# Kernel tuning notes

Hardware: AMD Instinct MI355X
Metric: run time of the kernel (lower is better)

## Reference

```python
import jax, jax.numpy as jnp
import numpy as np

E, H, V, B, T = 256, 512, 50257, 4, 512
EPS = 1e-5  # torch F.layer_norm default


def _ln(x):
    m = jnp.mean(x, axis=-1, keepdims=True)
    v = jnp.var(x, axis=-1, keepdims=True)
    return (x - m) / jnp.sqrt(v + EPS)


def setup_inputs() -> dict:
    key = jax.random.key(0)
    ks = iter(jax.random.split(key, 40))

    def w(shape):
        return jax.random.normal(next(ks), shape, dtype=jnp.float32) * 0.02

    inp = {"input_ids": jax.random.randint(next(ks), (B, T), 0, V)}
    inp["emb_table"] = w((V, E))
    for i, e in [(0, E), (1, H)]:  # layer 0 input = emb_dim, layer 1 input = hidden_dim
        inp[f"Wc1_{i}"] = w((2 * H + e, 2 * H)); inp[f"bc1_{i}"] = w((2 * H,))
        inp[f"Wc2_{i}"] = w((2 * H, H));         inp[f"bc2_{i}"] = w((H,))
        inp[f"Wg1_{i}"] = w((2 * H + e, H));     inp[f"bg1_{i}"] = w((H,))
        inp[f"Wg2_{i}"] = w((H, 1));             inp[f"bg2_{i}"] = w((1,))
        inp[f"Wr_{i}"] = w((e, H));              inp[f"br_{i}"] = w((H,))
    inp["Wa1"] = w((H, H)); inp["ba1"] = w((H,))
    inp["Wa2"] = w((H, 1)); inp["ba2"] = w((1,))
    inp["Wh"] = w((H, V));  inp["bh"] = w((V,))
    return inp


def _forward(input_ids, emb_table,
             Wc1_0, bc1_0, Wc2_0, bc2_0, Wg1_0, bg1_0, Wg2_0, bg2_0, Wr_0, br_0,
             Wc1_1, bc1_1, Wc2_1, bc2_1, Wg1_1, bg1_1, Wg2_1, bg2_1, Wr_1, br_1,
             Wa1, ba1, Wa2, ba2, Wh, bh):
    layers = [
        (Wc1_0, bc1_0, Wc2_0, bc2_0, Wg1_0, bg1_0, Wg2_0, bg2_0, Wr_0, br_0),
        (Wc1_1, bc1_1, Wc2_1, bc2_1, Wg1_1, bg1_1, Wg2_1, bg2_1, Wr_1, br_1),
    ]
    emb = emb_table[input_ids]  # [B,T,E]

    def step(carry, x_t):
        h2s, h1s = carry  # tuples of [B,H] per layer
        new_h2, new_h1 = [], []
        inp = x_t
        gate = None
        for (Wc1, bc1, Wc2, bc2, Wg1, bg1, Wg2, bg2, Wr, br), h2, h1 in zip(layers, h2s, h1s):
            ctx = jnp.concatenate([h1, h2, inp], axis=-1)  # [B, 2H+e]
            cand = jnp.maximum(ctx @ Wc1 + bc1, 0.0) @ Wc2 + bc2
            gate = jax.nn.sigmoid(jnp.tanh(ctx @ Wg1 + bg1) @ Wg2 + bg2)[:, 0]  # [B]
            h = _ln(h1 + gate[:, None] * cand + 0.1 * (inp @ Wr + br))
            new_h2.append(h1); new_h1.append(h)
            inp = h
        return (tuple(new_h2), tuple(new_h1)), (inp, gate)

    z = jnp.zeros((B, H), emb.dtype)
    init = ((z, z), (z, z))
    _, (hist, gates) = jax.lax.scan(step, init, jnp.swapaxes(emb, 0, 1))
    hist = jnp.swapaxes(hist, 0, 1)    # [B,T,H] last-layer hidden states
    gates = jnp.swapaxes(gates, 0, 1)  # [B,T]

    # Additive attention over the growing prefix: scores are fixed per position,
    # so prefix-softmax context = cumsum(exp(s)*h) / cumsum(exp(s)).
    scores = (jnp.tanh(hist @ Wa1 + ba1) @ Wa2 + ba2)[..., 0]  # [B,T]
    m = jnp.max(scores, axis=1, keepdims=True)
    e = jnp.exp(scores - m)
    num = jnp.cumsum(e[..., None] * hist, axis=1)  # [B,T,H]
    den = jnp.cumsum(e, axis=1)[..., None]
    attended = hist + num / den
    logits = attended @ Wh + bh  # [B,T,V]
    return logits, gates


def reference(input_ids, emb_table,
              Wc1_0, bc1_0, Wc2_0, bc2_0, Wg1_0, bg1_0, Wg2_0, bg2_0, Wr_0, br_0,
              Wc1_1, bc1_1, Wc2_1, bc2_1, Wg1_1, bg1_1, Wg2_1, bg2_1, Wr_1, br_1,
              Wa1, ba1, Wa2, ba2, Wh, bh):
    return _forward(input_ids, emb_table,
                    Wc1_0, bc1_0, Wc2_0, bc2_0, Wg1_0, bg1_0, Wg2_0, bg2_0, Wr_0, br_0,
                    Wc1_1, bc1_1, Wc2_1, bc2_1, Wg1_1, bg1_1, Wg2_1, bg2_1, Wr_1, br_1,
                    Wa1, ba1, Wa2, ba2, Wh, bh)
```

## Files before the change

### kernel.cpp

```cpp
#include <hip/hip_runtime.h>
#include <hip/hip_fp16.h>
#include <cstdint>
#include <cstddef>

typedef unsigned short u16;
typedef unsigned int   u32;
typedef unsigned long long u64;

#define Bn 4
#define Tn 512
#define Hn 512
#define En 256
#define Vn 50257
#define NPAD 50304
#define RG  256
#define RNT 256

typedef _Float16 h2t __attribute__((ext_vector_type(2)));

#if defined(__has_builtin)
#if __has_builtin(__builtin_amdgcn_fdot2)
#define HAS_FDOT2 1
#endif
#endif
__device__ __forceinline__ float fdot2f(h2t a, h2t b, float c) {
#ifdef HAS_FDOT2
  return __builtin_amdgcn_fdot2(a, b, c, false);
#else
  return fmaf((float)a[0], (float)b[0], fmaf((float)a[1], (float)b[1], c));
#endif
}

__device__ __forceinline__ u16 f2bf(float f) {
  u32 x; __builtin_memcpy(&x, &f, 4);
  u32 r = (x + 0x7fffu + ((x >> 16) & 1u)) >> 16;
  return (u16)r;
}
__device__ __forceinline__ u16 f2h(float f) {
  __half hh = __float2half(f); u16 u; __builtin_memcpy(&u, &hh, 2); return u;
}
__device__ __forceinline__ float h2fu(u16 h) {
  __half hh; __builtin_memcpy(&hh, &h, 2); return __half2float(hh);
}
__device__ __forceinline__ u64 gldu64(const u64* p) {
  return __hip_atomic_load(p, __ATOMIC_RELAXED, __HIP_MEMORY_SCOPE_AGENT);
}
__device__ __forceinline__ void gstu64(u64* p, u64 v) {
  __hip_atomic_store(p, v, __ATOMIC_RELAXED, __HIP_MEMORY_SCOPE_AGENT);
}
__device__ __forceinline__ u32 gldu32(const u32* p) {
  return __hip_atomic_load(p, __ATOMIC_RELAXED, __HIP_MEMORY_SCOPE_AGENT);
}
__device__ __forceinline__ void gstu32(u32* p, u32 v) {
  __hip_atomic_store(p, v, __ATOMIC_RELAXED, __HIP_MEMORY_SCOPE_AGENT);
}
__device__ __forceinline__ void gstf(float* p, float v) {
  __hip_atomic_store(p, v, __ATOMIC_RELAXED, __HIP_MEMORY_SCOPE_AGENT);
}

__global__ __launch_bounds__(256) void transpose_h(
    const float* __restrict__ src, __half* __restrict__ dst, int K, int N)
{
  __shared__ float tile[32][33];
  const int tx = threadIdx.x & 31, ty = threadIdx.x >> 5;
  const int bn = blockIdx.x * 32, bk = blockIdx.y * 32;
  #pragma unroll
  for (int i = 0; i < 4; ++i)
    tile[ty + i * 8][tx] = src[(size_t)(bk + ty + i * 8) * N + bn + tx];
  __syncthreads();
  #pragma unroll
  for (int i = 0; i < 4; ++i)
    dst[(size_t)(bn + ty + i * 8) * K + bk + tx] = __float2half(tile[tx][ty + i * 8]);
}

__global__ __launch_bounds__(256) void convwh_kernel(
    const float* __restrict__ wh, u16* __restrict__ whb)
{
  const int k = blockIdx.y;
  const int v0 = (blockIdx.x * 256 + threadIdx.x) * 2;
  if (v0 >= NPAD) return;
  float a = (v0     < Vn) ? wh[(size_t)k * Vn + v0]     : 0.f;
  float b = (v0 + 1 < Vn) ? wh[(size_t)k * Vn + v0 + 1] : 0.f;
  u32 pack = (u32)f2bf(a) | ((u32)f2bf(b) << 16);
  *(u32*)&whb[(size_t)k * NPAD + v0] = pack;
}

#define HR16_B  98304
#define HR0_B   102400
#define EMB_B   104448
#define XCAND_B 105472
#define GP_B    109568
#define RLOC_B  110080
#define SS_B    110144
#define BC1L_B  110464
#define BG1L_B  110528
#define BC2L_B  110560
#define BRL_B   110592
#define WG2L_B  110624
#define BG2L_B  110656
#define REC_LDS 110720

__global__ __launch_bounds__(RNT, 1) void rec_kernel(
    const int* __restrict__ ids, const float* __restrict__ emb,
    const __half* wtC1_0, const __half* wtG1_0, const __half* wtC2_0, const __half* wtR_0,
    const __half* wtC1_1, const __half* wtG1_1, const __half* wtC2_1, const __half* wtR_1,
    const float* bc1_0, const float* bg1_0, const float* bc2_0, const float* br_0,
    const float* wg2_0, const float* bg2_0,
    const float* bc1_1, const float* bg1_1, const float* bc2_1, const float* br_1,
    const float* wg2_1, const float* bg2_1,
    u32* flagA, u64* HB, u64* CB,
    float* __restrict__ histN, float* __restrict__ gates_out)
{
  extern __shared__ char smem[];
  __half* WL    = (__half*)smem;
  __half* hr16  = (__half*)(smem + HR16_B);
  __half* hr0   = (__half*)(smem + HR0_B);
  __half* emb16 = (__half*)(smem + EMB_B);
  __half* xcand = (__half*)(smem + XCAND_B);
  float* gp     = (float*)(smem + GP_B);
  float* rloc   = (float*)(smem + RLOC_B);
  float* Ss     = (float*)(smem + SS_B);
  float* bc1L   = (float*)(smem + BC1L_B);
  float* bg1L   = (float*)(smem + BG1L_B);
  float* bc2L   = (float*)(smem + BC2L_B);
  float* brL    = (float*)(smem + BRL_B);
  float* wg2L   = (float*)(smem + WG2L_B);
  float* bg2L   = (float*)(smem + BG2L_B);

  const int tid = threadIdx.x, g = blockIdx.x;
  const int bp = g >> 7, l = (g >> 6) & 1, gl = g & 63;
  const int w = tid >> 6, lane = tid & 63;
  const int C = l ? 1536 : 1280;
  const int e = l ? 512 : 256;
  const int oG1 = 16 * C, oR = 24 * C, oC2 = 24 * C + 8 * e;

  const __half* wtC1 = l ? wtC1_1 : wtC1_0;
  const __half* wtG1 = l ? wtG1_1 : wtG1_0;
  const __half* wtC2 = l ? wtC2_1 : wtC2_0;
  const __half* wtR  = l ? wtR_1  : wtR_0;
  const float* bc1 = l ? bc1_1 : bc1_0;
  const float* bg1 = l ? bg1_1 : bg1_0;
  const float* bc2 = l ? bc2_1 : bc2_0;
  const float* br  = l ? br_1  : br_0;
  const float* wg2 = l ? wg2_1 : wg2_0;
  const float* bg2 = l ? bg2_1 : bg2_0;

  u64* HBown = HB + (size_t)((bp * 2 + l) * 2) * 512;
  u64* CBown = CB + (size_t)((bp * 2 + l) * 2) * 1152;
  const u64* HBl0 = HB + (size_t)((bp * 2) * 2) * 512;

  {
    auto cp = [&](const __half* src, int nh, int offh) {
      const u32* s = (const u32*)src; u32* d = (u32*)(WL + offh);
      for (int i = tid; i < (nh >> 1); i += RNT) d[i] = s[i];
    };
    cp(wtC1 + (size_t)(gl * 16) * C, 16 * C, 0);
    cp(wtG1 + (size_t)(gl * 8) * C,  8 * C, oG1);
    cp(wtR  + (size_t)(gl * 8) * e,  8 * e, oR);
    cp(wtC2 + (size_t)(gl * 8) * 1024, 8 * 1024, oC2);
  }
  for (int i = tid; i < 2960; i += RNT) ((u32*)(smem + HR16_B))[i] = 0;
  __syncthreads();

  if (tid < 16)      bc1L[tid] = bc1[gl * 16 + tid];
  else if (tid < 24) bg1L[tid - 16] = bg1[gl * 8 + tid - 16];
  else if (tid < 32) bc2L[tid - 24] = bc2[gl * 8 + tid - 24];
  else if (tid < 40) brL[tid - 32]  = br[gl * 8 + tid - 32];
  else if (tid < 48) wg2L[tid - 40] = wg2[gl * 8 + tid - 40];
  else if (tid == 48) bg2L[0] = bg2[0];
  for (int task = w; task < 32; task += 4) {
    const __half* colp; int K;
    if (task < 16)      { colp = WL + (size_t)task * C;              K = C; }
    else if (task < 24) { colp = WL + oG1 + (size_t)(task - 16) * C; K = C; }
    else                { colp = WL + oR  + (size_t)(task - 24) * e; K = e; }
    float s1 = 0.f, s2 = 0.f, s3 = 0.f;
    for (int k = lane; k < K; k += 64) {
      float v = __half2float(colp[k]);
      if (K == e) s1 += v;
      else if (k < 512) s1 += v;
      else if (k < 1024) s2 += v;
      else s3 += v;
    }
    #pragma unroll
    for (int off = 32; off; off >>= 1) {
      s1 += __shfl_xor(s1, off); s2 += __shfl_xor(s2, off); s3 += __shfl_xor(s3, off);
    }
    if (lane == 0) {
      if (task < 16)      { Ss[task] = s1; Ss[16 + task] = s2; Ss[32 + task] = s3; }
      else if (task < 24) { Ss[48 + task - 16] = s1; Ss[56 + task - 16] = s2; Ss[64 + task - 16] = s3; }
      else                { Ss[72 + task - 24] = s1; }
    }
  }
  __syncthreads();

  const int nEnd = l ? (Tn + 1) : (Tn - 1);
  float mp[2] = {0.f, 0.f}, ipv[2] = {0.f, 0.f};

  for (int n = 0; n <= nEnd; ++n) {
    const int t = n - l;
    const bool prod = (t >= 0) && (t < Tn);
    const bool pollOwn = (t >= 1) && (t <= Tn);
    const bool pollL0  = (l == 1) && prod;
    const int parR = (n - 1) & 1;

    float2 e2 = make_float2(0.f, 0.f);
    if (l == 0 && prod) {
      int idv = ids[(bp * 2 + (w >> 1)) * Tn + t];
      e2 = *(const float2*)(emb + (size_t)idv * En + (tid & 127) * 2);
    }

    if (pollOwn || pollL0) {
      const u64* s1 = HBown + (size_t)parR * 512;
      const u64* s0 = HBl0 + (size_t)parR * 512;
      const u32 want = (u32)n;
      u64 v1[2], v0[2];
      for (;;) {
        bool ok = true;
        if (pollOwn) { v1[0] = gldu64(s1 + tid); v1[1] = gldu64(s1 + 256 + tid); }
        if (pollL0)  { v0[0] = gldu64(s0 + tid); v0[1] = gldu64(s0 + 256 + tid); }
        if (pollOwn) ok &= ((u32)(v1[0] >> 32) == want) & ((u32)(v1[1] >> 32) == want);
        if (pollL0)  ok &= ((u32)(v0[0] >> 32) == want) & ((u32)(v0[1] >> 32) == want);
        if (ok) break;
        __builtin_amdgcn_s_sleep(1);
      }
      if (pollOwn) {
        #pragma unroll
        for (int i = 0; i < 2; ++i) {
          int W = i * 256 + tid;
          int glp = W >> 3, q = W & 7, cpp = q >> 1, b = q & 1;
          ((u32*)(hr16 + (parR * 2 + b) * 512))[glp * 4 + cpp] = (u32)v1[i];
        }
      }
      if (pollL0) {
        #pragma unroll
        for (int i = 0; i < 2; ++i) {
          int W = i * 256 + tid;
          int glp = W >> 3, q = W & 7, cpp = q >> 1, b = q & 1;
          ((u32*)(hr0 + b * 512))[glp * 4 + cpp] = (u32)v0[i];
        }
      }
    }
    if (l == 0 && prod) {
      u32 pp = (u32)f2h(e2.x) | ((u32)f2h(e2.y) << 16);
      ((u32*)emb16)[(w >> 1) * 128 + (tid & 127)] = pp;
    }
    __syncthreads();
    if (l == 1 && tid == 0) gstu32(flagA + (bp * 64 + gl) * 16, (u32)(n + 1));

    float m1[2] = {0.f, 0.f}, i1v[2] = {0.f, 0.f};
    float m3[2] = {0.f, 0.f}, i3v[2] = {0.f, 0.f};
    if (pollOwn) {
      float s[2] = {0.f, 0.f}, q[2] = {0.f, 0.f};
      #pragma unroll
      for (int b = 0; b < 2; ++b) {
        const u32* hp = (const u32*)(hr16 + (parR * 2 + b) * 512);
        #pragma unroll
        for (int i2 = 0; i2 < 4; ++i2) {
          u32 vv = hp[lane + i2 * 64];
          __half2 hh; __builtin_memcpy(&hh, &vv, 4);
          float2 f2 = __half22float2(hh);
          s[b] += f2.x + f2.y; q[b] += f2.x * f2.x + f2.y * f2.y;
        }
      }
      #pragma unroll
      for (int off = 32; off; off >>= 1) {
        s[0] += __shfl_xor(s[0], off); q[0] += __shfl_xor(q[0], off);
        s[1] += __shfl_xor(s[1], off); q[1] += __shfl_xor(q[1], off);
      }
      #pragma unroll
      for (int b = 0; b < 2; ++b) {
        float m = s[b] * (1.f / 512.f);
        m1[b] = m; i1v[b] = rsqrtf(q[b] * (1.f / 512.f) - m * m + 1e-5f);
      }
    }
    if (pollL0) {
      float s[2] = {0.f, 0.f}, q[2] = {0.f, 0.f};
      #pragma unroll
      for (int b = 0; b < 2; ++b) {
        const u32* hp = (const u32*)(hr0 + b * 512);
        #pragma unroll
        for (int i2 = 0; i2 < 4; ++i2) {
          u32 vv = hp[lane + i2 * 64];
          __half2 hh; __builtin_memcpy(&hh, &vv, 4);
          float2 f2 = __half22float2(hh);
          s[b] += f2.x + f2.y; q[b] += f2.x * f2.x + f2.y * f2.y;
        }
      }
      #pragma unroll
      for (int off = 32; off; off >>= 1) {
        s[0] += __shfl_xor(s[0], off); q[0] += __shfl_xor(q[0], off);
        s[1] += __shfl_xor(s[1], off); q[1] += __shfl_xor(q[1], off);
      }
      #pragma unroll
      for (int b = 0; b < 2; ++b) {
        float m = s[b] * (1.f / 512.f);
        m3[b] = m; i3v[b] = rsqrtf(q[b] * (1.f / 512.f) - m * m + 1e-5f);
      }
    }

    if (l == 1 && pollOwn && tid < 16) {
      int c = tid >> 1, b = tid & 1, j = gl * 8 + c;
      float rv = __half2float(hr16[(parR * 2 + b) * 512 + j]);
      gstf(histN + ((size_t)((bp * 2 + b) * Tn + (t - 1))) * Hn + j, (rv - m1[b]) * i1v[b]);
    }

    if (prod) {
      float comb[8][2];
      #pragma unroll
      for (int c = 0; c < 8; ++c) { comb[c][0] = 0.f; comb[c][1] = 0.f; }
      const __half* h1p[2] = { hr16 + (parR * 2) * 512, hr16 + (parR * 2 + 1) * 512 };
      const __half* h2p[2] = { hr16 + ((parR ^ 1) * 2) * 512, hr16 + ((parR ^ 1) * 2 + 1) * 512 };
      float a[8][2];

      if (w < 3) {
        const __half* wbase = (w < 2) ? (WL + (size_t)(w * 8) * C) : (WL + oG1);
        #pragma unroll
        for (int c = 0; c < 8; ++c) { a[c][0] = 0.f; a[c][1] = 0.f; }
        #pragma unroll
        for (int it = 0; it < 4; ++it) {
          int p2 = lane + it * 64;
          h2t x0 = *(const h2t*)(h1p[0] + 2 * p2);
          h2t x1 = *(const h2t*)(h1p[1] + 2 * p2);
          #pragma unroll
          for (int c = 0; c < 8; ++c) {
            h2t wv = *(const h2t*)(wbase + (size_t)c * C + 2 * p2);
            a[c][0] = fdot2f(wv, x0, a[c][0]);
            a[c][1] = fdot2f(wv, x1, a[c][1]);
          }
        }
        #pragma unroll
        for (int c = 0; c < 8; ++c) { comb[c][0] += i1v[0] * a[c][0]; comb[c][1] += i1v[1] * a[c][1]; }
        #pragma unroll
        for (int c = 0; c < 8; ++c) { a[c][0] = 0.f; a[c][1] = 0.f; }
        #pragma unroll
        for (int it = 0; it < 4; ++it) {
          int p2 = lane + it * 64;
          h2t x0 = *(const h2t*)(h2p[0] + 2 * p2);
          h2t x1 = *(const h2t*)(h2p[1] + 2 * p2);
          #pragma unroll
          for (int c = 0; c < 8; ++c) {
            h2t wv = *(const h2t*)(wbase + (size_t)c * C + 512 + 2 * p2);
            a[c][0] = fdot2f(wv, x0, a[c][0]);
            a[c][1] = fdot2f(wv, x1, a[c][1]);
          }
        }
        #pragma unroll
        for (int c = 0; c < 8; ++c) { comb[c][0] += ipv[0] * a[c][0]; comb[c][1] += ipv[1] * a[c][1]; }
        #pragma unroll
        for (int c = 0; c < 8; ++c) { a[c][0] = 0.f; a[c][1] = 0.f; }
        if (l == 0) {
          #pragma unroll
          for (int it = 0; it < 2; ++it) {
            int p2 = lane + it * 64;
            h2t x0 = *(const h2t*)(emb16 + 2 * p2);
            h2t x1 = *(const h2t*)(emb16 + 256 + 2 * p2);
            #pragma unroll
            for (int c = 0; c < 8; ++c) {
              h2t wv = *(const h2t*)(wbase + (size_t)c * C + 1024 + 2 * p2);
              a[c][0] = fdot2f(wv, x0, a[c][0]);
              a[c][1] = fdot2f(wv, x1, a[c][1]);
            }
          }
          #pragma unroll
          for (int c = 0; c < 8; ++c) { comb[c][0] += a[c][0]; comb[c][1] += a[c][1]; }
        } else {
          #pragma unroll
          for (int it = 0; it < 4; ++it) {
            int p2 = lane + it * 64;
            h2t x0 = *(const h2t*)(hr0 + 2 * p2);
            h2t x1 = *(const h2t*)(hr0 + 512 + 2 * p2);
            #pragma unroll
            for (int c = 0; c < 8; ++c) {
              h2t wv = *(const h2t*)(wbase + (size_t)c * C + 1024 + 2 * p2);
              a[c][0] = fdot2f(wv, x0, a[c][0]);
              a[c][1] = fdot2f(wv, x1, a[c][1]);
            }
          }
          #pragma unroll
          for (int c = 0; c < 8; ++c) { comb[c][0] += i3v[0] * a[c][0]; comb[c][1] += i3v[1] * a[c][1]; }
        }
      } else {
        #pragma unroll
        for (int c = 0; c < 8; ++c) { a[c][0] = 0.f; a[c][1] = 0.f; }
        if (l == 0) {
          #pragma unroll
          for (int it = 0; it < 2; ++it) {
            int p2 = lane + it * 64;
            h2t x0 = *(const h2t*)(emb16 + 2 * p2);
            h2t x1 = *(const h2t*)(emb16 + 256 + 2 * p2);
            #pragma unroll
            for (int c = 0; c < 8; ++c) {
              h2t wv = *(const h2t*)(WL + oR + (size_t)c * e + 2 * p2);
              a[c][0] = fdot2f(wv, x0, a[c][0]);
              a[c][1] = fdot2f(wv, x1, a[c][1]);
            }
          }
          #pragma unroll
          for (int c = 0; c < 8; ++c) { comb[c][0] = a[c][0]; comb[c][1] = a[c][1]; }
        } else {
          #pragma unroll
          for (int it = 0; it < 4; ++it) {
            int p2 = lane + it * 64;
            h2t x0 = *(const h2t*)(hr0 + 2 * p2);
            h2t x1 = *(const h2t*)(hr0 + 512 + 2 * p2);
            #pragma unroll
            for (int c = 0; c < 8; ++c) {
              h2t wv = *(const h2t*)(WL + oR + (size_t)c * e + 2 * p2);
              a[c][0] = fdot2f(wv, x0, a[c][0]);
              a[c][1] = fdot2f(wv, x1, a[c][1]);
            }
          }
          #pragma unroll
          for (int c = 0; c < 8; ++c) { comb[c][0] = i3v[0] * a[c][0]; comb[c][1] = i3v[1] * a[c][1]; }
        }
      }
      #pragma unroll
      for (int off = 32; off; off >>= 1)
        #pragma unroll
        for (int c = 0; c < 8; ++c) {
          comb[c][0] += __shfl_xor(comb[c][0], off);
          comb[c][1] += __shfl_xor(comb[c][1], off);
        }
      float v0s = 0.f, v1s = 0.f;
      #pragma unroll
      for (int c = 0; c < 8; ++c)
        if (lane == c) { v0s = comb[c][0]; v1s = comb[c][1]; }

      const u64 tagw = ((u64)(u32)(n + 1)) << 32;
      u64* CBw = CBown + (size_t)(n & 1) * 1152 + gl * 18;
      if (w < 2) {
        if (lane < 8) {
          int cg = w * 8 + lane;
          float k0 = i1v[0] * m1[0] * Ss[cg] + ipv[0] * mp[0] * Ss[16 + cg];
          float k1 = i1v[1] * m1[1] * Ss[cg] + ipv[1] * mp[1] * Ss[16 + cg];
          if (l) { k0 += i3v[0] * m3[0] * Ss[32 + cg]; k1 += i3v[1] * m3[1] * Ss[32 + cg]; }
          float bb = bc1L[cg];
          float c0 = fmaxf(v0s - k0 + bb, 0.f), c1 = fmaxf(v1s - k1 + bb, 0.f);
          u32 pay = (u32)f2h(c0) | ((u32)f2h(c1) << 16);
          gstu64(CBw + cg, tagw | pay);
        }
      } else if (w == 2) {
        if (lane < 8) {
          float k0 = i1v[0] * m1[0] * Ss[48 + lane] + ipv[0] * mp[0] * Ss[56 + lane];
          float k1 = i1v[1] * m1[1] * Ss[48 + lane] + ipv[1] * mp[1] * Ss[56 + lane];
          if (l) { k0 += i3v[0] * m3[0] * Ss[64 + lane]; k1 += i3v[1] * m3[1] * Ss[64 + lane]; }
          float bgv = bg1L[lane], wgv = wg2L[lane];
          float t0 = tanhf(v0s - k0 + bgv) * wgv;
          float t1 = tanhf(v1s - k1 + bgv) * wgv;
          #pragma unroll
          for (int off = 1; off < 8; off <<= 1) { t0 += __shfl_xor(t0, off); t1 += __shfl_xor(t1, off); }
          if (lane == 0) {
            u32 b0, b1; __builtin_memcpy(&b0, &t0, 4); __builtin_memcpy(&b1, &t1, 4);
            gstu64(CBw + 16, tagw | b0);
            gstu64(CBw + 17, tagw | b1);
          }
        }
      } else {
        if (lane < 8) {
          float k0 = l ? i3v[0] * m3[0] * Ss[72 + lane] : 0.f;
          float k1 = l ? i3v[1] * m3[1] * Ss[72 + lane] : 0.f;
          rloc[lane * 2]     = v0s - k0 + brL[lane];
          rloc[lane * 2 + 1] = v1s - k1 + brL[lane];
        }
      }
    }

    if (prod) {
      const u64* CBL = CBown + (size_t)(n & 1) * 1152;
      const u32 want = (u32)(n + 1);
      const bool needF = (l == 0) && (tid < 64);
      const u32* fptr = flagA + (bp * 64 + tid) * 16;
      u64 cv[5];
      const bool last = (tid < 128);
      for (;;) {
        bool ok = true;
        #pragma unroll
        for (int i = 0; i < 4; ++i) cv[i] = gldu64(CBL + i * 256 + tid);
        if (last) cv[4] = gldu64(CBL + 1024 + tid);
        #pragma unroll
        for (int i = 0; i < 4; ++i) ok &= ((u32)(cv[i] >> 32) == want);
        if (last) ok &= ((u32)(cv[4] >> 32) == want);
        if (needF) ok &= (gldu32(fptr) >= (u32)n);
        if (ok) break;
        __builtin_amdgcn_s_sleep(1);
      }
      u16* xc16 = (u16*)xcand;
      #pragma unroll
      for (int i = 0; i < 5; ++i) {
        if (i == 4 && !last) break;
        int idx = i * 256 + tid;
        int p = (int)(((u32)idx * 3641u) >> 16);
        int w2 = idx - p * 18;
        u32 pay = (u32)cv[i];
        if (w2 < 16) {
          int j = p * 16 + w2;
          xc16[j]        = (u16)(pay & 0xffffu);
          xc16[1024 + j] = (u16)(pay >> 16);
        } else {
          float f; __builtin_memcpy(&f, &pay, 4);
          gp[p * 2 + (w2 - 16)] = f;
        }
      }
    }
    __syncthreads();

    if (prod) {
      float gs0 = gp[lane * 2], gs1 = gp[lane * 2 + 1];
      #pragma unroll
      for (int off = 32; off; off >>= 1) { gs0 += __shfl_xor(gs0, off); gs1 += __shfl_xor(gs1, off); }
      float gate[2];
      gate[0] = 1.f / (1.f + expf(-(gs0 + bg2L[0])));
      gate[1] = 1.f / (1.f + expf(-(gs1 + bg2L[0])));

      float a2[2][2];
      a2[0][0] = a2[0][1] = a2[1][0] = a2[1][1] = 0.f;
      const __half* wb2 = WL + oC2 + (w * 2) * 1024;
      #pragma unroll
      for (int it = 0; it < 8; ++it) {
        int p2 = lane + it * 64;
        h2t xv0 = *(const h2t*)(xcand + 2 * p2);
        h2t xv1 = *(const h2t*)(xcand + 1024 + 2 * p2);
        #pragma unroll
        for (int cc = 0; cc < 2; ++cc) {
          h2t wv = *(const h2t*)(wb2 + cc * 1024 + 2 * p2);
          a2[cc][0] = fdot2f(wv, xv0, a2[cc][0]);
          a2[cc][1] = fdot2f(wv, xv1, a2[cc][1]);
        }
      }
      #pragma unroll
      for (int off = 32; off; off >>= 1)
        #pragma unroll
        for (int cc = 0; cc < 2; ++cc) {
          a2[cc][0] += __shfl_xor(a2[cc][0], off);
          a2[cc][1] += __shfl_xor(a2[cc][1], off);
        }
      float sel = 0.f;
      #pragma unroll
      for (int cc = 0; cc < 2; ++cc)
        #pragma unroll
        for (int b = 0; b < 2; ++b)
          if (lane == cc * 2 + b) sel = a2[cc][b];
      int cc = (lane >> 1) & 1, b = lane & 1, cl = w * 2 + cc;
      float rv = __half2float(hr16[(parR * 2 + b) * 512 + gl * 8 + cl]);
      float h1n = (rv - m1[b]) * i1v[b];
      float hv = h1n + gate[b] * (sel + bc2L[cl]) + 0.1f * rloc[cl * 2 + b];
      float hv0 = __shfl(hv, 0), hv1 = __shfl(hv, 1);
      float hv2 = __shfl(hv, 2), hv3 = __shfl(hv, 3);
      if (lane < 2) {
        u32 pay = (lane == 0) ? ((u32)f2h(hv0) | ((u32)f2h(hv2) << 16))
                              : ((u32)f2h(hv1) | ((u32)f2h(hv3) << 16));
        u64* HBw = HBown + (size_t)(n & 1) * 512 + gl * 8;
        gstu64(HBw + w * 2 + lane, (((u64)(u32)(n + 1)) << 32) | pay);
      }
      if (l == 1 && gl == 0 && w == 0 && lane == 0) {
        gstf(gates_out + (bp * 2) * Tn + t, gate[0]);
        gstf(gates_out + (bp * 2 + 1) * Tn + t, gate[1]);
      }
    }

    if (pollOwn) { mp[0] = m1[0]; mp[1] = m1[1]; ipv[0] = i1v[0]; ipv[1] = i1v[1]; }
  }
}

__global__ __launch_bounds__(256) void scores_kernel(
    const float* __restrict__ histN,
    const float* __restrict__ wa1, const float* __restrict__ ba1,
    const float* __restrict__ wa2, const float* __restrict__ ba2,
    float* __restrict__ scores)
{
  __shared__ float xs[8][512];
  __shared__ float wacc[4][8];
  const int tid = threadIdx.x, bid = blockIdx.x;

  for (int idx = tid; idx < 4096; idx += 256)
    xs[idx >> 9][idx & 511] = histN[(size_t)(bid * 8) * Hn + idx];
  __syncthreads();

  float pr[8] = {0.f,0.f,0.f,0.f,0.f,0.f,0.f,0.f};
  #pragma unroll
  for (int cc = 0; cc < 2; ++cc) {
    int c = tid + cc * 256;
    float a[8] = {0.f,0.f,0.f,0.f,0.f,0.f,0.f,0.f};
    for (int k = 0; k < 512; ++k) {
      float wv = wa1[(size_t)k * 512 + c];
      #pragma unroll
      for (int r = 0; r < 8; ++r) a[r] = fmaf(xs[r][k], wv, a[r]);
    }
    float b1 = ba1[c], w2 = wa2[c];
    #pragma unroll
    for (int r = 0; r < 8; ++r) pr[r] += tanhf(a[r] + b1) * w2;
  }
  int lane = tid & 63, wq = tid >> 6;
  #pragma unroll
  for (int off = 32; off; off >>= 1)
    #pragma unroll
    for (int r = 0; r < 8; ++r) pr[r] += __shfl_xor(pr[r], off);
  if (lane == 0) {
    #pragma unroll
    for (int r = 0; r < 8; ++r) wacc[wq][r] = pr[r];
  }
  __syncthreads();
  if (tid < 8)
    scores[bid * 8 + tid] = wacc[0][tid] + wacc[1][tid] + wacc[2][tid] + wacc[3][tid] + ba2[0];
}

__global__ __launch_bounds__(256) void cumsum_scan_kernel(
    const float* __restrict__ scores, const float* __restrict__ histN,
    u16* __restrict__ att)
{
  __shared__ float ee[512], sa[512], sb[512], red[256];
  __shared__ float tile[64][64];
  const int tid = threadIdx.x;
  const int b = blockIdx.y, j0 = blockIdx.x * 64;

  float s0 = scores[b * Tn + tid], s1 = scores[b * Tn + tid + 256];
  red[tid] = fmaxf(s0, s1);
  __syncthreads();
  for (int s = 128; s; s >>= 1) { if (tid < s) red[tid] = fmaxf(red[tid], red[tid + s]); __syncthreads(); }
  float m = red[0];
  ee[tid] = expf(s0 - m); ee[tid + 256] = expf(s1 - m);
  sa[tid] = ee[tid]; sa[tid + 256] = ee[tid + 256];
  __syncthreads();
  float* A = sa; float* D = sb;
  for (int off = 1; off < 512; off <<= 1) {
    for (int t2 = tid; t2 < 512; t2 += 256) { float v = A[t2]; if (t2 >= off) v += A[t2 - off]; D[t2] = v; }
    __syncthreads();
    float* tmp = A; A = D; D = tmp;
  }
  float* R = D;
  for (int t2 = tid; t2 < 512; t2 += 256) R[t2] = 1.f / A[t2];
  __syncthreads();

  float ax = 0.f;
  for (int tt = 0; tt < 8; ++tt) {
    #pragma unroll
    for (int k = 0; k < 16; ++k) {
      int idx = tid + k * 256;
      int r = idx >> 6, c = idx & 63;
      tile[r][c] = histN[(size_t)(b * Tn + tt * 64 + r) * Hn + j0 + c];
    }
    __syncthreads();
    if (tid < 64) {
      for (int r = 0; r < 64; ++r) {
        int t = tt * 64 + r;
        float x = tile[r][tid];
        ax = fmaf(ee[t], x, ax);
        att[((size_t)(b * Tn + t)) * Hn + j0 + tid] = f2bf(x + ax * R[t]);
      }
    }
    __syncthreads();
  }
}

typedef short bf16x8_t __attribute__((ext_vector_type(8)));
typedef float f32x4_t  __attribute__((ext_vector_type(4)));

__global__ __launch_bounds__(256) void gemm_kernel(
    const u16* __restrict__ Aw, const u16* __restrict__ Bw,
    const float* __restrict__ bh, float* __restrict__ out)
{
  __shared__ u16 Alds[128 * 64];
  __shared__ u16 Blds[64 * 128];
  const int tid = threadIdx.x;
  const int n0 = blockIdx.x * 128, m0 = blockIdx.y * 128;
  const int w = tid >> 6, lane = tid & 63;
  const int wm = (w & 1) * 64, wn = (w >> 1) * 64;

  f32x4_t acc[4][4];
  #pragma unroll
  for (int i = 0; i < 4; ++i)
    #pragma unroll
    for (int j = 0; j < 4; ++j) acc[i][j] = (f32x4_t){0.f, 0.f, 0.f, 0.f};

  for (int kt = 0; kt < 8; ++kt) {
    const int k0 = kt * 64;
    {
      int row = tid >> 1, kc = (tid & 1) * 32;
      #pragma unroll
      for (int jj = 0; jj < 4; ++jj) {
        uint4 v = *(const uint4*)(Aw + (size_t)(m0 + row) * 512 + k0 + kc + jj * 8);
        int byte = row * 128 + (kc + jj * 8) * 2;
        byte ^= (row & 7) << 4;
        *(uint4*)((char*)Alds + byte) = v;
      }
    }
    {
      #pragma unroll
      for (int q = 0; q < 4; ++q) {
        int r = (tid >> 4) + q * 16, c8 = (tid & 15) * 8;
        uint4 v = *(const uint4*)(Bw + (size_t)(k0 + r) * NPAD + n0 + c8);
        *(uint4*)&Blds[r * 128 + c8] = v;
      }
    }
    __syncthreads();
    #pragma unroll
    for (int kh = 0; kh < 2; ++kh) {
      bf16x8_t af[4];
      #pragma unroll
      for (int i = 0; i < 4; ++i) {
        int row = wm + i * 16 + (lane & 15);
        int byte = row * 128 + kh * 64 + (lane >> 4) * 16;
        byte ^= (row & 7) << 4;
        af[i] = *(const bf16x8_t*)((const char*)Alds + byte);
      }
      const int kb = kh * 32 + (lane >> 4) * 8;
      #pragma unroll
      for (int j = 0; j < 4; ++j) {
        int col = wn + j * 16 + (lane & 15);
        bf16x8_t bf;
        #pragma unroll
        for (int jj = 0; jj < 8; ++jj) bf[jj] = (short)Blds[(kb + jj) * 128 + col];
        #pragma unroll
        for (int i = 0; i < 4; ++i)
          acc[i][j] = __builtin_amdgcn_mfma_f32_16x16x32_bf16(af[i], bf, acc[i][j], 0, 0, 0);
      }
    }
    __syncthreads();
  }
  #pragma unroll
  for (int j = 0; j < 4; ++j) {
    int col = n0 + wn + j * 16 + (lane & 15);
    if (col < Vn) {
      float bias = bh[col];
      #pragma unroll
      for (int i = 0; i < 4; ++i) {
        int rbase = m0 + wm + i * 16 + (lane >> 4) * 4;
        #pragma unroll
        for (int r = 0; r < 4; ++r)
          out[(size_t)(rbase + r) * Vn + col] = acc[i][j][r] + bias;
      }
    }
  }
}

extern "C" void kernel_launch(void* const* d_in, const int* in_sizes, int n_in,
                              void* d_out, int out_size, void* d_ws, size_t ws_size,
                              hipStream_t stream) {
  const int*   ids  = (const int*)d_in[0];
  const float* emb  = (const float*)d_in[1];
  const float* Wc1_0 = (const float*)d_in[2];  const float* bc1_0 = (const float*)d_in[3];
  const float* Wc2_0 = (const float*)d_in[4];  const float* bc2_0 = (const float*)d_in[5];
  const float* Wg1_0 = (const float*)d_in[6];  const float* bg1_0 = (const float*)d_in[7];
  const float* Wg2_0 = (const float*)d_in[8];  const float* bg2_0 = (const float*)d_in[9];
  const float* Wr_0  = (const float*)d_in[10]; const float* br_0  = (const float*)d_in[11];
  const float* Wc1_1 = (const float*)d_in[12]; const float* bc1_1 = (const float*)d_in[13];
  const float* Wc2_1 = (const float*)d_in[14]; const float* bc2_1 = (const float*)d_in[15];
  const float* Wg1_1 = (const float*)d_in[16]; const float* bg1_1 = (const float*)d_in[17];
  const float* Wg2_1 = (const float*)d_in[18]; const float* bg2_1 = (const float*)d_in[19];
  const float* Wr_1  = (const float*)d_in[20]; const float* br_1  = (const float*)d_in[21];
  const float* Wa1 = (const float*)d_in[22]; const float* ba1 = (const float*)d_in[23];
  const float* Wa2 = (const float*)d_in[24]; const float* ba2 = (const float*)d_in[25];
  const float* Wh  = (const float*)d_in[26]; const float* bh  = (const float*)d_in[27];

  float* out = (float*)d_out;
  char*  ws  = (char*)d_ws;

  const size_t OFF_FLAGA = 0;
  const size_t OFF_HB    = 8192;
  const size_t OFF_CB    = 40960;
  const size_t OFF_WT    = 114688;
  const size_t OFF_HISTN = OFF_WT + 11534336;
  const size_t OFF_SCO   = OFF_HISTN + 4194304;
  const size_t OFF_ATT   = OFF_SCO + 8192;
  const size_t OFF_WHB   = OFF_ATT + 2097152;

  u32*   flagA  = (u32*)(ws + OFF_FLAGA);
  u64*   HB     = (u64*)(ws + OFF_HB);
  u64*   CB     = (u64*)(ws + OFF_CB);
  __half* wth   = (__half*)(ws + OFF_WT);
  float* histN  = (float*)(ws + OFF_HISTN);
  float* scores = (float*)(ws + OFF_SCO);
  u16*   att    = (u16*)(ws + OFF_ATT);
  u16*   whb    = (u16*)(ws + OFF_WHB);
  float* gates  = out + (size_t)Bn * Tn * Vn;

  __half* wtC1_0h = wth;
  __half* wtG1_0h = wth + 1310720;
  __half* wtC2_0h = wth + 1966080;
  __half* wtR_0h  = wth + 2490368;
  __half* wtC1_1h = wth + 2621440;
  __half* wtG1_1h = wth + 4194304;
  __half* wtC2_1h = wth + 4980736;
  __half* wtR_1h  = wth + 5505024;

  hipMemsetAsync(ws, 0, 114688, stream);

  transpose_h<<<dim3(32, 40), 256, 0, stream>>>(Wc1_0, wtC1_0h, 1280, 1024);
  transpose_h<<<dim3(16, 40), 256, 0, stream>>>(Wg1_0, wtG1_0h, 1280, 512);
  transpose_h<<<dim3(16, 32), 256, 0, stream>>>(Wc2_0, wtC2_0h, 1024, 512);
  transpose_h<<<dim3(16,  8), 256, 0, stream>>>(Wr_0,  wtR_0h,   256, 512);
  transpose_h<<<dim3(32, 48), 256, 0, stream>>>(Wc1_1, wtC1_1h, 1536, 1024);
  transpose_h<<<dim3(16, 48), 256, 0, stream>>>(Wg1_1, wtG1_1h, 1536, 512);
  transpose_h<<<dim3(16, 32), 256, 0, stream>>>(Wc2_1, wtC2_1h, 1024, 512);
  transpose_h<<<dim3(16, 16), 256, 0, stream>>>(Wr_1,  wtR_1h,   512, 512);

  convwh_kernel<<<dim3(99, 512), 256, 0, stream>>>(Wh, whb);

  (void)hipFuncSetAttribute((const void*)rec_kernel,
                            hipFuncAttributeMaxDynamicSharedMemorySize, REC_LDS);

  rec_kernel<<<dim3(RG), dim3(RNT), REC_LDS, stream>>>(
      ids, emb,
      wtC1_0h, wtG1_0h, wtC2_0h, wtR_0h,
      wtC1_1h, wtG1_1h, wtC2_1h, wtR_1h,
      bc1_0, bg1_0, bc2_0, br_0, Wg2_0, bg2_0,
      bc1_1, bg1_1, bc2_1, br_1, Wg2_1, bg2_1,
      flagA, HB, CB, histN, gates);

  scores_kernel<<<dim3(256), 256, 0, stream>>>(histN, Wa1, ba1, Wa2, ba2, scores);

  cumsum_scan_kernel<<<dim3(8, Bn), 256, 0, stream>>>(scores, histN, att);

  gemm_kernel<<<dim3(393, 16), 256, 0, stream>>>(att, whb, bh, out);
}
```

Before: 4.522 ms.

## Precompute h2 and embedding dot products before polling for new hidden state

```diff
diff --git a/kernel.cpp b/kernel.cpp
--- a/kernel.cpp
+++ b/kernel.cpp
@@ -38,9 +38,6 @@
 }
 __device__ __forceinline__ u16 f2h(float f) {
   __half hh = __float2half(f); u16 u; __builtin_memcpy(&u, &hh, 2); return u;
-}
-__device__ __forceinline__ float h2fu(u16 h) {
-  __half hh; __builtin_memcpy(&hh, &h, 2); return __half2float(hh);
 }
 __device__ __forceinline__ u64 gldu64(const u64* p) {
   return __hip_atomic_load(p, __ATOMIC_RELAXED, __HIP_MEMORY_SCOPE_AGENT);
@@ -98,7 +95,9 @@
 #define BRL_B   110592
 #define WG2L_B  110624
 #define BG2L_B  110656
-#define REC_LDS 110720
+#define STW_B   110720
+#define STW0_B  110784
+#define REC_LDS 110848
 
 __global__ __launch_bounds__(RNT, 1) void rec_kernel(
     const int* __restrict__ ids, const float* __restrict__ emb,
@@ -115,7 +114,6 @@
   __half* WL    = (__half*)smem;
   __half* hr16  = (__half*)(smem + HR16_B);
   __half* hr0   = (__half*)(smem + HR0_B);
-  __half* emb16 = (__half*)(smem + EMB_B);
   __half* xcand = (__half*)(smem + XCAND_B);
   float* gp     = (float*)(smem + GP_B);
   float* rloc   = (float*)(smem + RLOC_B);
@@ -126,6 +124,8 @@
   float* brL    = (float*)(smem + BRL_B);
   float* wg2L   = (float*)(smem + WG2L_B);
   float* bg2L   = (float*)(smem + BG2L_B);
+  float* stw    = (float*)(smem + STW_B);
+  float* stw0   = (float*)(smem + STW0_B);
 
   const int tid = threadIdx.x, g = blockIdx.x;
   const int bp = g >> 7, l = (g >> 6) & 1, gl = g & 63;
@@ -203,10 +203,78 @@
     const bool pollL0  = (l == 1) && prod;
     const int parR = (n - 1) & 1;
 
-    float2 e2 = make_float2(0.f, 0.f);
+    h2t er0[2], er1[2];
+    er0[0] = (h2t)0; er0[1] = (h2t)0; er1[0] = (h2t)0; er1[1] = (h2t)0;
     if (l == 0 && prod) {
-      int idv = ids[(bp * 2 + (w >> 1)) * Tn + t];
-      e2 = *(const float2*)(emb + (size_t)idv * En + (tid & 127) * 2);
+      int id0 = ids[(bp * 2) * Tn + t];
+      int id1 = ids[(bp * 2 + 1) * Tn + t];
+      float2 fa0 = *(const float2*)(emb + (size_t)id0 * En + 2 * lane);
+      float2 fb0 = *(const float2*)(emb + (size_t)id0 * En + 2 * (lane + 64));
+      float2 fa1 = *(const float2*)(emb + (size_t)id1 * En + 2 * lane);
+      float2 fb1 = *(const float2*)(emb + (size_t)id1 * En + 2 * (lane + 64));
+      er0[0][0] = (_Float16)fa0.x; er0[0][1] = (_Float16)fa0.y;
+      er0[1][0] = (_Float16)fb0.x; er0[1][1] = (_Float16)fb0.y;
+      er1[0][0] = (_Float16)fa1.x; er1[0][1] = (_Float16)fa1.y;
+      er1[1][0] = (_Float16)fb1.x; er1[1][1] = (_Float16)fb1.y;
+    }
+
+    float comb[8][2];
+    #pragma unroll
+    for (int c = 0; c < 8; ++c) { comb[c][0] = 0.f; comb[c][1] = 0.f; }
+    if (prod) {
+      const __half* h2pl[2] = { hr16 + ((parR ^ 1) * 2) * 512,
+                                hr16 + ((parR ^ 1) * 2 + 1) * 512 };
+      float a[8][2];
+      if (w < 3) {
+        const __half* wbase = (w < 2) ? (WL + (size_t)(w * 8) * C) : (WL + oG1);
+        #pragma unroll
+        for (int c = 0; c < 8; ++c) { a[c][0] = 0.f; a[c][1] = 0.f; }
+        #pragma unroll
+        for (int it = 0; it < 4; ++it) {
+          int p2 = lane + it * 64;
+          h2t x0 = *(const h2t*)(h2pl[0] + 2 * p2);
+          h2t x1 = *(const h2t*)(h2pl[1] + 2 * p2);
+          #pragma unroll
+          for (int c = 0; c < 8; ++c) {
+            h2t wv = *(const h2t*)(wbase + (size_t)c * C + 512 + 2 * p2);
+            a[c][0] = fdot2f(wv, x0, a[c][0]);
+            a[c][1] = fdot2f(wv, x1, a[c][1]);
+          }
+        }
+        #pragma unroll
+        for (int c = 0; c < 8; ++c) { comb[c][0] += ipv[0] * a[c][0]; comb[c][1] += ipv[1] * a[c][1]; }
+        if (l == 0) {
+          #pragma unroll
+          for (int c = 0; c < 8; ++c) { a[c][0] = 0.f; a[c][1] = 0.f; }
+          #pragma unroll
+          for (int it = 0; it < 2; ++it) {
+            int p2 = lane + it * 64;
+            #pragma unroll
+            for (int c = 0; c < 8; ++c) {
+              h2t wv = *(const h2t*)(wbase + (size_t)c * C + 1024 + 2 * p2);
+              a[c][0] = fdot2f(wv, er0[it], a[c][0]);
+              a[c][1] = fdot2f(wv, er1[it], a[c][1]);
+            }
+          }
+          #pragma unroll
+          for (int c = 0; c < 8; ++c) { comb[c][0] += a[c][0]; comb[c][1] += a[c][1]; }
+        }
+      } else if (l == 0) {
+        #pragma unroll
+        for (int c = 0; c < 8; ++c) { a[c][0] = 0.f; a[c][1] = 0.f; }
+        #pragma unroll
+        for (int it = 0; it < 2; ++it) {
+          int p2 = lane + it * 64;
+          #pragma unroll
+          for (int c = 0; c < 8; ++c) {
+            h2t wv = *(const h2t*)(WL + oR + (size_t)c * e + 2 * p2);
+            a[c][0] = fdot2f(wv, er0[it], a[c][0]);
+            a[c][1] = fdot2f(wv, er1[it], a[c][1]);
+          }
+        }
+        #pragma unroll
+        for (int c = 0; c < 8; ++c) { comb[c][0] = a[c][0]; comb[c][1] = a[c][1]; }
+      }
     }
 
     if (pollOwn || pollL0) {
@@ -221,28 +289,48 @@
         if (pollOwn) ok &= ((u32)(v1[0] >> 32) == want) & ((u32)(v1[1] >> 32) == want);
         if (pollL0)  ok &= ((u32)(v0[0] >> 32) == want) & ((u32)(v0[1] >> 32) == want);
         if (ok) break;
-        __builtin_amdgcn_s_sleep(1);
+        __builtin_amdgcn_s_sleep(2);
       }
       if (pollOwn) {
+        float sb0 = 0.f, sb1 = 0.f, qb0 = 0.f, qb1 = 0.f;
         #pragma unroll
         for (int i = 0; i < 2; ++i) {
           int W = i * 256 + tid;
           int glp = W >> 3, q = W & 7, cpp = q >> 1, b = q & 1;
-          ((u32*)(hr16 + (parR * 2 + b) * 512))[glp * 4 + cpp] = (u32)v1[i];
-        }
+          u32 pay = (u32)v1[i];
+          ((u32*)(hr16 + (parR * 2 + b) * 512))[glp * 4 + cpp] = pay;
+          __half2 hh; __builtin_memcpy(&hh, &pay, 4);
+          float2 fv = __half22float2(hh);
+          float sv = fv.x + fv.y, qv = fv.x * fv.x + fv.y * fv.y;
+          if (b == 0) { sb0 += sv; qb0 += qv; } else { sb1 += sv; qb1 += qv; }
+        }
+        #pragma unroll
+        for (int off = 32; off; off >>= 1) {
+          sb0 += __shfl_xor(sb0, off); qb0 += __shfl_xor(qb0, off);
+          sb1 += __shfl_xor(sb1, off); qb1 += __shfl_xor(qb1, off);
+        }
+        if (lane == 0) { stw[w * 4] = sb0; stw[w * 4 + 1] = sb1; stw[w * 4 + 2] = qb0; stw[w * 4 + 3] = qb1; }
       }
       if (pollL0) {
+        float sb0 = 0.f, sb1 = 0.f, qb0 = 0.f, qb1 = 0.f;
         #pragma unroll
         for (int i = 0; i < 2; ++i) {
           int W = i * 256 + tid;
           int glp = W >> 3, q = W & 7, cpp = q >> 1, b = q & 1;
-          ((u32*)(hr0 + b * 512))[glp * 4 + cpp] = (u32)v0[i];
-        }
-      }
-    }
-    if (l == 0 && prod) {
-      u32 pp = (u32)f2h(e2.x) | ((u32)f2h(e2.y) << 16);
-      ((u32*)emb16)[(w >> 1) * 128 + (tid & 127)] = pp;
+          u32 pay = (u32)v0[i];
+          ((u32*)(hr0 + b * 512))[glp * 4 + cpp] = pay;
+          __half2 hh; __builtin_memcpy(&hh, &pay, 4);
+          float2 fv = __half22float2(hh);
+          float sv = fv.x + fv.y, qv = fv.x * fv.x + fv.y * fv.y;
+          if (b == 0) { sb0 += sv; qb0 += qv; } else { sb1 += sv; qb1 += qv; }
+        }
+        #pragma unroll
+        for (int off = 32; off; off >>= 1) {
+          sb0 += __shfl_xor(sb0, off); qb0 += __shfl_xor(qb0, off);
+          sb1 += __shfl_xor(sb1, off); qb1 += __shfl_xor(qb1, off);
+        }
+        if (lane == 0) { stw0[w * 4] = sb0; stw0[w * 4 + 1] = sb1; stw0[w * 4 + 2] = qb0; stw0[w * 4 + 3] = qb1; }
+      }
     }
     __syncthreads();
     if (l == 1 && tid == 0) gstu32(flagA + (bp * 64 + gl) * 16, (u32)(n + 1));
@@ -250,52 +338,20 @@
     float m1[2] = {0.f, 0.f}, i1v[2] = {0.f, 0.f};
     float m3[2] = {0.f, 0.f}, i3v[2] = {0.f, 0.f};
     if (pollOwn) {
-      float s[2] = {0.f, 0.f}, q[2] = {0.f, 0.f};
-      #pragma unroll
-      for (int b = 0; b < 2; ++b) {
-        const u32* hp = (const u32*)(hr16 + (parR * 2 + b) * 512);
-        #pragma unroll
-        for (int i2 = 0; i2 < 4; ++i2) {
-          u32 vv = hp[lane + i2 * 64];
-          __half2 hh; __builtin_memcpy(&hh, &vv, 4);
-          float2 f2 = __half22float2(hh);
-          s[b] += f2.x + f2.y; q[b] += f2.x * f2.x + f2.y * f2.y;
-        }
-      }
-      #pragma unroll
-      for (int off = 32; off; off >>= 1) {
-        s[0] += __shfl_xor(s[0], off); q[0] += __shfl_xor(q[0], off);
-        s[1] += __shfl_xor(s[1], off); q[1] += __shfl_xor(q[1], off);
-      }
-      #pragma unroll
-      for (int b = 0; b < 2; ++b) {
-        float m = s[b] * (1.f / 512.f);
-        m1[b] = m; i1v[b] = rsqrtf(q[b] * (1.f / 512.f) - m * m + 1e-5f);
-      }
+      float S0 = stw[0] + stw[4] + stw[8] + stw[12];
+      float S1 = stw[1] + stw[5] + stw[9] + stw[13];
+      float Q0 = stw[2] + stw[6] + stw[10] + stw[14];
+      float Q1 = stw[3] + stw[7] + stw[11] + stw[15];
+      m1[0] = S0 * (1.f / 512.f); i1v[0] = rsqrtf(Q0 * (1.f / 512.f) - m1[0] * m1[0] + 1e-5f);
+      m1[1] = S1 * (1.f / 512.f); i1v[1] = rsqrtf(Q1 * (1.f / 512.f) - m1[1] * m1[1] + 1e-5f);
     }
     if (pollL0) {
-      float s[2] = {0.f, 0.f}, q[2] = {0.f, 0.f};
-      #pragma unroll
-      for (int b = 0; b < 2; ++b) {
-        const u32* hp = (const u32*)(hr0 + b * 512);
-        #pragma unroll
-        for (int i2 = 0; i2 < 4; ++i2) {
-          u32 vv = hp[lane + i2 * 64];
-          __half2 hh; __builtin_memcpy(&hh, &vv, 4);
-          float2 f2 = __half22float2(hh);
-          s[b] += f2.x + f2.y; q[b] += f2.x * f2.x + f2.y * f2.y;
-        }
-      }
-      #pragma unroll
-      for (int off = 32; off; off >>= 1) {
-        s[0] += __shfl_xor(s[0], off); q[0] += __shfl_xor(q[0], off);
-        s[1] += __shfl_xor(s[1], off); q[1] += __shfl_xor(q[1], off);
-      }
-      #pragma unroll
-      for (int b = 0; b < 2; ++b) {
-        float m = s[b] * (1.f / 512.f);
-        m3[b] = m; i3v[b] = rsqrtf(q[b] * (1.f / 512.f) - m * m + 1e-5f);
-      }
+      float S0 = stw0[0] + stw0[4] + stw0[8] + stw0[12];
+      float S1 = stw0[1] + stw0[5] + stw0[9] + stw0[13];
+      float Q0 = stw0[2] + stw0[6] + stw0[10] + stw0[14];
+      float Q1 = stw0[3] + stw0[7] + stw0[11] + stw0[15];
+      m3[0] = S0 * (1.f / 512.f); i3v[0] = rsqrtf(Q0 * (1.f / 512.f) - m3[0] * m3[0] + 1e-5f);
+      m3[1] = S1 * (1.f / 512.f); i3v[1] = rsqrtf(Q1 * (1.f / 512.f) - m3[1] * m3[1] + 1e-5f);
     }
 
     if (l == 1 && pollOwn && tid < 16) {
@@ -305,13 +361,8 @@
     }
 
     if (prod) {
-      float comb[8][2];
-      #pragma unroll
-      for (int c = 0; c < 8; ++c) { comb[c][0] = 0.f; comb[c][1] = 0.f; }
-      const __half* h1p[2] = { hr16 + (parR * 2) * 512, hr16 + (parR * 2 + 1) * 512 };
-      const __half* h2p[2] = { hr16 + ((parR ^ 1) * 2) * 512, hr16 + ((parR ^ 1) * 2 + 1) * 512 };
+      const __half* h1pl[2] = { hr16 + (parR * 2) * 512, hr16 + (parR * 2 + 1) * 512 };
       float a[8][2];
-
       if (w < 3) {
         const __half* wbase = (w < 2) ? (WL + (size_t)(w * 8) * C) : (WL + oG1);
         #pragma unroll
@@ -319,8 +370,8 @@
         #pragma unroll
         for (int it = 0; it < 4; ++it) {
           int p2 = lane + it * 64;
-          h2t x0 = *(const h2t*)(h1p[0] + 2 * p2);
-          h2t x1 = *(const h2t*)(h1p[1] + 2 * p2);
+          h2t x0 = *(const h2t*)(h1pl[0] + 2 * p2);
+          h2t x1 = *(const h2t*)(h1pl[1] + 2 * p2);
           #pragma unroll
           for (int c = 0; c < 8; ++c) {
             h2t wv = *(const h2t*)(wbase + (size_t)c * C + 2 * p2);
@@ -330,40 +381,9 @@
         }
         #pragma unroll
         for (int c = 0; c < 8; ++c) { comb[c][0] += i1v[0] * a[c][0]; comb[c][1] += i1v[1] * a[c][1]; }
-        #pragma unroll
-        for (int c = 0; c < 8; ++c) { a[c][0] = 0.f; a[c][1] = 0.f; }
-        #pragma unroll
-        for (int it = 0; it < 4; ++it) {
-          int p2 = lane + it * 64;
-          h2t x0 = *(const h2t*)(h2p[0] + 2 * p2);
-          h2t x1 = *(const h2t*)(h2p[1] + 2 * p2);
-          #pragma unroll
-          for (int c = 0; c < 8; ++c) {
-            h2t wv = *(const h2t*)(wbase + (size_t)c * C + 512 + 2 * p2);
-            a[c][0] = fdot2f(wv, x0, a[c][0]);
-            a[c][1] = fdot2f(wv, x1, a[c][1]);
-          }
-        }
-        #pragma unroll
-        for (int c = 0; c < 8; ++c) { comb[c][0] += ipv[0] * a[c][0]; comb[c][1] += ipv[1] * a[c][1]; }
-        #pragma unroll
-        for (int c = 0; c < 8; ++c) { a[c][0] = 0.f; a[c][1] = 0.f; }
-        if (l == 0) {
-          #pragma unroll
-          for (int it = 0; it < 2; ++it) {
-            int p2 = lane + it * 64;
-            h2t x0 = *(const h2t*)(emb16 + 2 * p2);
-            h2t x1 = *(const h2t*)(emb16 + 256 + 2 * p2);
-            #pragma unroll
-            for (int c = 0; c < 8; ++c) {
-              h2t wv = *(const h2t*)(wbase + (size_t)c * C + 1024 + 2 * p2);
-              a[c][0] = fdot2f(wv, x0, a[c][0]);
-              a[c][1] = fdot2f(wv, x1, a[c][1]);
-            }
-          }
-          #pragma unroll
-          for (int c = 0; c < 8; ++c) { comb[c][0] += a[c][0]; comb[c][1] += a[c][1]; }
-        } else {
+        if (l == 1) {
+          #pragma unroll
+          for (int c = 0; c < 8; ++c) { a[c][0] = 0.f; a[c][1] = 0.f; }
           #pragma unroll
           for (int it = 0; it < 4; ++it) {
             int p2 = lane + it * 64;
@@ -379,41 +399,25 @@
           #pragma unroll
           for (int c = 0; c < 8; ++c) { comb[c][0] += i3v[0] * a[c][0]; comb[c][1] += i3v[1] * a[c][1]; }
         }
-      } else {
+      } else if (l == 1) {
         #pragma unroll
         for (int c = 0; c < 8; ++c) { a[c][0] = 0.f; a[c][1] = 0.f; }
-        if (l == 0) {
-          #pragma unroll
-          for (int it = 0; it < 2; ++it) {
-            int p2 = lane + it * 64;
-            h2t x0 = *(const h2t*)(emb16 + 2 * p2);
-            h2t x1 = *(const h2t*)(emb16 + 256 + 2 * p2);
-            #pragma unroll
-            for (int c = 0; c < 8; ++c) {
-              h2t wv = *(const h2t*)(WL + oR + (size_t)c * e + 2 * p2);
-              a[c][0] = fdot2f(wv, x0, a[c][0]);
-              a[c][1] = fdot2f(wv, x1, a[c][1]);
-            }
+        #pragma unroll
+        for (int it = 0; it < 4; ++it) {
+          int p2 = lane + it * 64;
+          h2t x0 = *(const h2t*)(hr0 + 2 * p2);
+          h2t x1 = *(const h2t*)(hr0 + 512 + 2 * p2);
+          #pragma unroll
+          for (int c = 0; c < 8; ++c) {
+            h2t wv = *(const h2t*)(WL + oR + (size_t)c * e + 2 * p2);
+            a[c][0] = fdot2f(wv, x0, a[c][0]);
+            a[c][1] = fdot2f(wv, x1, a[c][1]);
           }
-          #pragma unroll
-          for (int c = 0; c < 8; ++c) { comb[c][0] = a[c][0]; comb[c][1] = a[c][1]; }
-        } else {
-          #pragma unroll
-          for (int it = 0; it < 4; ++it) {
-            int p2 = lane + it * 64;
-            h2t x0 = *(const h2t*)(hr0 + 2 * p2);
-            h2t x1 = *(const h2t*)(hr0 + 512 + 2 * p2);
-            #pragma unroll
-            for (int c = 0; c < 8; ++c) {
-              h2t wv = *(const h2t*)(WL + oR + (size_t)c * e + 2 * p2);
-              a[c][0] = fdot2f(wv, x0, a[c][0]);
-              a[c][1] = fdot2f(wv, x1, a[c][1]);
-            }
-          }
-          #pragma unroll
-          for (int c = 0; c < 8; ++c) { comb[c][0] = i3v[0] * a[c][0]; comb[c][1] = i3v[1] * a[c][1]; }
-        }
-      }
+        }
+        #pragma unroll
+        for (int c = 0; c < 8; ++c) { comb[c][0] = i3v[0] * a[c][0]; comb[c][1] = i3v[1] * a[c][1]; }
+      }
+
       #pragma unroll
       for (int off = 32; off; off >>= 1)
         #pragma unroll
@@ -482,7 +486,7 @@
         if (last) ok &= ((u32)(cv[4] >> 32) == want);
         if (needF) ok &= (gldu32(fptr) >= (u32)n);
         if (ok) break;
-        __builtin_amdgcn_s_sleep(1);
+        __builtin_amdgcn_s_sleep(2);
       }
       u16* xc16 = (u16*)xcand;
       #pragma unroll
```

Result: faster. 4.331 ms (-4.2%).
